# Optimization experiments

Hardware: AMD Instinct MI355X
Metric: run time of the kernel (lower is better)

Reference implementation:

```python
import jax, jax.numpy as jnp
from jax import lax
import numpy as np

N_BITS = 108
N_OUT = 7
# pos_bits[i, j] = bit j (MSB-first) of index i, matching `i >> (6 - j) & 1`
POS_BITS = np.array([[(i >> (6 - j)) & 1 for j in range(N_OUT)] for i in range(N_BITS)], dtype=np.float32)
# LZC value when all 108 bits are zero: 108 = 1101100b, MSB first
LZC_108 = np.array([1, 1, 0, 1, 1, 0, 0], dtype=np.float32)


def setup_inputs() -> dict:
    key = jax.random.key(0)
    # sparse binary bits so leading-zero runs are long and some rows are all-zero
    X = (jax.random.uniform(key, (2_000_000, N_BITS)) < 0.03).astype(jnp.float32)
    return {"X": X}


def _lzd(X):
    """X: [..., 108] MSB-first bits -> [..., 7] LZC MSB-first.

    Arithmetic soft-gate semantics: NOT(a)=1-a, AND(a,b)=a*b,
    OR(a,b)=a+b-a*b, MUX(s,a,b)=s*a+(1-s)*b, OR-tree = 1-prod(1-x).
    Sequential carry over `found` expressed with lax.scan (108 steps).
    """
    batch_shape = X.shape[:-1]
    bits = jnp.moveaxis(X, -1, 0)  # [108, ...]
    pos = jnp.asarray(POS_BITS, dtype=X.dtype)  # [108, 7]

    def step(carry, inp):
        found, lzc = carry                  # found: [..., 1], lzc: [..., 7]
        bit, pos_bits = inp                 # bit: [...], pos_bits: [7]
        bit = bit[..., None]                # [..., 1]
        not_found = 1.0 - found             # NOT
        is_first = bit * not_found          # AND
        # MUX per output bit: is_first ? pos_bit : lzc
        lzc = is_first * pos_bits + (1.0 - is_first) * lzc
        # OR: found | is_first
        found = found + is_first - found * is_first
        return (found, lzc), None

    found0 = jnp.zeros(batch_shape + (1,), X.dtype)
    lzc0 = jnp.zeros(batch_shape + (N_OUT,), X.dtype)
    (found, lzc), _ = lax.scan(step, (found0, lzc0), (bits, pos))

    # OR-tree over all 108 bits, then all-zero override with LZC=108
    any_one = 1.0 - jnp.prod(1.0 - X, axis=-1, keepdims=True)  # [..., 1]
    all_zero = 1.0 - any_one                                   # NOT
    lzc108 = jnp.asarray(LZC_108, dtype=X.dtype)               # [7]
    return all_zero * lzc108 + (1.0 - all_zero) * lzc


def reference(X):
    return _lzd(X)
```

## Files before the change

### kernel.cpp

```cpp
#include <hip/hip_runtime.h>


#define LZD_NBITS 108
#define LZD_NOUT 7

__global__ __launch_bounds__(256) void lzd108_kernel(const float* __restrict__ X,
                                                     float* __restrict__ out,
                                                     int n_rows) {
    int row = blockIdx.x * blockDim.x + threadIdx.x;
    if (row >= n_rows) return;

    const float4* p = reinterpret_cast<const float4*>(X + (size_t)row * LZD_NBITS);

    int idx = -1;

    #pragma unroll 1
    for (int c = 0; c < 6; ++c) {
        float4 v0 = p[4 * c + 0];
        float4 v1 = p[4 * c + 1];
        float4 v2 = p[4 * c + 2];
        float4 v3 = p[4 * c + 3];
        unsigned m = 0u;
        m |= (v0.x != 0.0f) ? (1u << 0)  : 0u;
        m |= (v0.y != 0.0f) ? (1u << 1)  : 0u;
        m |= (v0.z != 0.0f) ? (1u << 2)  : 0u;
        m |= (v0.w != 0.0f) ? (1u << 3)  : 0u;
        m |= (v1.x != 0.0f) ? (1u << 4)  : 0u;
        m |= (v1.y != 0.0f) ? (1u << 5)  : 0u;
        m |= (v1.z != 0.0f) ? (1u << 6)  : 0u;
        m |= (v1.w != 0.0f) ? (1u << 7)  : 0u;
        m |= (v2.x != 0.0f) ? (1u << 8)  : 0u;
        m |= (v2.y != 0.0f) ? (1u << 9)  : 0u;
        m |= (v2.z != 0.0f) ? (1u << 10) : 0u;
        m |= (v2.w != 0.0f) ? (1u << 11) : 0u;
        m |= (v3.x != 0.0f) ? (1u << 12) : 0u;
        m |= (v3.y != 0.0f) ? (1u << 13) : 0u;
        m |= (v3.z != 0.0f) ? (1u << 14) : 0u;
        m |= (v3.w != 0.0f) ? (1u << 15) : 0u;
        if (m) {
            idx = 16 * c + (__ffs(m) - 1);
            break;
        }
    }

    if (idx < 0) {
        float4 v0 = p[24];
        float4 v1 = p[25];
        float4 v2 = p[26];
        unsigned m = 0u;
        m |= (v0.x != 0.0f) ? (1u << 0)  : 0u;
        m |= (v0.y != 0.0f) ? (1u << 1)  : 0u;
        m |= (v0.z != 0.0f) ? (1u << 2)  : 0u;
        m |= (v0.w != 0.0f) ? (1u << 3)  : 0u;
        m |= (v1.x != 0.0f) ? (1u << 4)  : 0u;
        m |= (v1.y != 0.0f) ? (1u << 5)  : 0u;
        m |= (v1.z != 0.0f) ? (1u << 6)  : 0u;
        m |= (v1.w != 0.0f) ? (1u << 7)  : 0u;
        m |= (v2.x != 0.0f) ? (1u << 8)  : 0u;
        m |= (v2.y != 0.0f) ? (1u << 9)  : 0u;
        m |= (v2.z != 0.0f) ? (1u << 10) : 0u;
        m |= (v2.w != 0.0f) ? (1u << 11) : 0u;
        idx = m ? (96 + (__ffs(m) - 1)) : LZD_NBITS;
    }

    float* o = out + (size_t)row * LZD_NOUT;
    o[0] = (float)((idx >> 6) & 1);
    o[1] = (float)((idx >> 5) & 1);
    o[2] = (float)((idx >> 4) & 1);
    o[3] = (float)((idx >> 3) & 1);
    o[4] = (float)((idx >> 2) & 1);
    o[5] = (float)((idx >> 1) & 1);
    o[6] = (float)(idx & 1);
}

extern "C" void kernel_launch(void* const* d_in, const int* in_sizes, int n_in,
                              void* d_out, int out_size, void* d_ws, size_t ws_size,
                              hipStream_t stream) {
    const float* X = (const float*)d_in[0];
    float* out = (float*)d_out;
    int n_rows = in_sizes[0] / LZD_NBITS;
    int block = 256;
    int grid = (n_rows + block - 1) / block;
    lzd108_kernel<<<grid, block, 0, stream>>>(X, out, n_rows);
}
```

Baseline: 1.027 ms.

## Coalesce row loads via block-cooperative float4 reads and shared-memory key reduction

Each block now reads its 256 rows as one contiguous stream of float4s, so adjacent threads load adjacent addresses. Each float4 is turned into a 16-bit first-set-position key in shared memory, and each thread then takes the minimum over its row's 27 keys. The old version had each thread stride through its own row with early exit, which gave uncoalesced access. The new version gives up early exit and always reads all 108 bits, in exchange for full coalescing.

New measurement: 1.116 ms. +8.7%, slower.

```diff
diff --git a/kernel.cpp b/kernel.cpp
--- a/kernel.cpp
+++ b/kernel.cpp
@@ -3,74 +3,79 @@
 
 #define LZD_NBITS 108
 #define LZD_NOUT 7
+#define RPB 256
+#define F4R 27
+#define F4B (RPB * F4R)
+#define KPAD 28
+
+static __device__ __forceinline__ unsigned umin_(unsigned a, unsigned b) {
+    return a < b ? a : b;
+}
 
 __global__ __launch_bounds__(256) void lzd108_kernel(const float* __restrict__ X,
                                                      float* __restrict__ out,
                                                      int n_rows) {
-    int row = blockIdx.x * blockDim.x + threadIdx.x;
-    if (row >= n_rows) return;
+    __shared__ unsigned short keys[RPB][KPAD];
+    const int tid = threadIdx.x;
+    const size_t row0 = (size_t)blockIdx.x * RPB;
+    const float4* __restrict__ p =
+        reinterpret_cast<const float4*>(X) + row0 * F4R;
 
-    const float4* p = reinterpret_cast<const float4*>(X + (size_t)row * LZD_NBITS);
+    keys[tid][F4R] = (unsigned short)0xFFFFu;
 
-    int idx = -1;
+    const size_t nf4_rem = ((size_t)n_rows - row0) * F4R;
 
-    #pragma unroll 1
-    for (int c = 0; c < 6; ++c) {
-        float4 v0 = p[4 * c + 0];
-        float4 v1 = p[4 * c + 1];
-        float4 v2 = p[4 * c + 2];
-        float4 v3 = p[4 * c + 3];
-        unsigned m = 0u;
-        m |= (v0.x != 0.0f) ? (1u << 0)  : 0u;
-        m |= (v0.y != 0.0f) ? (1u << 1)  : 0u;
-        m |= (v0.z != 0.0f) ? (1u << 2)  : 0u;
-        m |= (v0.w != 0.0f) ? (1u << 3)  : 0u;
-        m |= (v1.x != 0.0f) ? (1u << 4)  : 0u;
-        m |= (v1.y != 0.0f) ? (1u << 5)  : 0u;
-        m |= (v1.z != 0.0f) ? (1u << 6)  : 0u;
-        m |= (v1.w != 0.0f) ? (1u << 7)  : 0u;
-        m |= (v2.x != 0.0f) ? (1u << 8)  : 0u;
-        m |= (v2.y != 0.0f) ? (1u << 9)  : 0u;
-        m |= (v2.z != 0.0f) ? (1u << 10) : 0u;
-        m |= (v2.w != 0.0f) ? (1u << 11) : 0u;
-        m |= (v3.x != 0.0f) ? (1u << 12) : 0u;
-        m |= (v3.y != 0.0f) ? (1u << 13) : 0u;
-        m |= (v3.z != 0.0f) ? (1u << 14) : 0u;
-        m |= (v3.w != 0.0f) ? (1u << 15) : 0u;
-        if (m) {
-            idx = 16 * c + (__ffs(m) - 1);
-            break;
+    if (nf4_rem >= (size_t)F4B) {
+        #pragma unroll
+        for (int it = 0; it < F4B / RPB; ++it) {
+            const int i = tid + it * RPB;
+            const float4 v = p[i];
+            const int r = i / F4R;
+            const int c = i - r * F4R;
+            const unsigned sub = (v.x != 0.0f) ? 0u
+                               : (v.y != 0.0f) ? 1u
+                               : (v.z != 0.0f) ? 2u
+                               : (v.w != 0.0f) ? 3u : 4u;
+            keys[r][c] = (sub == 4u) ? (unsigned short)0xFFFFu
+                                     : (unsigned short)(4u * (unsigned)c + sub);
+        }
+    } else {
+        const int nf4 = (int)nf4_rem;
+        #pragma unroll 1
+        for (int i = tid; i < nf4; i += RPB) {
+            const float4 v = p[i];
+            const int r = i / F4R;
+            const int c = i - r * F4R;
+            const unsigned sub = (v.x != 0.0f) ? 0u
+                               : (v.y != 0.0f) ? 1u
+                               : (v.z != 0.0f) ? 2u
+                               : (v.w != 0.0f) ? 3u : 4u;
+            keys[r][c] = (sub == 4u) ? (unsigned short)0xFFFFu
+                                     : (unsigned short)(4u * (unsigned)c + sub);
         }
     }
+    __syncthreads();
 
-    if (idx < 0) {
-        float4 v0 = p[24];
-        float4 v1 = p[25];
-        float4 v2 = p[26];
-        unsigned m = 0u;
-        m |= (v0.x != 0.0f) ? (1u << 0)  : 0u;
-        m |= (v0.y != 0.0f) ? (1u << 1)  : 0u;
-        m |= (v0.z != 0.0f) ? (1u << 2)  : 0u;
-        m |= (v0.w != 0.0f) ? (1u << 3)  : 0u;
-        m |= (v1.x != 0.0f) ? (1u << 4)  : 0u;
-        m |= (v1.y != 0.0f) ? (1u << 5)  : 0u;
-        m |= (v1.z != 0.0f) ? (1u << 6)  : 0u;
-        m |= (v1.w != 0.0f) ? (1u << 7)  : 0u;
-        m |= (v2.x != 0.0f) ? (1u << 8)  : 0u;
-        m |= (v2.y != 0.0f) ? (1u << 9)  : 0u;
-        m |= (v2.z != 0.0f) ? (1u << 10) : 0u;
-        m |= (v2.w != 0.0f) ? (1u << 11) : 0u;
-        idx = m ? (96 + (__ffs(m) - 1)) : LZD_NBITS;
+    const size_t row = row0 + (size_t)tid;
+    if (row < (size_t)n_rows) {
+        const uint2* kp = reinterpret_cast<const uint2*>(&keys[tid][0]);
+        unsigned m = 0xFFFFu;
+        #pragma unroll
+        for (int j = 0; j < 7; ++j) {
+            const uint2 u = kp[j];
+            m = umin_(m, umin_(umin_(u.x & 0xFFFFu, u.x >> 16),
+                               umin_(u.y & 0xFFFFu, u.y >> 16)));
+        }
+        const unsigned idx = (m > 107u) ? (unsigned)LZD_NBITS : m;
+        float* o = out + row * LZD_NOUT;
+        o[0] = (float)((idx >> 6) & 1u);
+        o[1] = (float)((idx >> 5) & 1u);
+        o[2] = (float)((idx >> 4) & 1u);
+        o[3] = (float)((idx >> 3) & 1u);
+        o[4] = (float)((idx >> 2) & 1u);
+        o[5] = (float)((idx >> 1) & 1u);
+        o[6] = (float)(idx & 1u);
     }
-
-    float* o = out + (size_t)row * LZD_NOUT;
-    o[0] = (float)((idx >> 6) & 1);
-    o[1] = (float)((idx >> 5) & 1);
-    o[2] = (float)((idx >> 4) & 1);
-    o[3] = (float)((idx >> 3) & 1);
-    o[4] = (float)((idx >> 2) & 1);
-    o[5] = (float)((idx >> 1) & 1);
-    o[6] = (float)(idx & 1);
 }
 
 extern "C" void kernel_launch(void* const* d_in, const int* in_sizes, int n_in,
@@ -80,6 +85,6 @@
     float* out = (float*)d_out;
     int n_rows = in_sizes[0] / LZD_NBITS;
     int block = 256;
-    int grid = (n_rows + block - 1) / block;
+    int grid = (n_rows + RPB - 1) / RPB;
     lzd108_kernel<<<grid, block, 0, stream>>>(X, out, n_rows);
 }
```

## Issue 16 aligned 128B-segment loads upfront and extract bits from exponent

Applied to the files above, without the earlier changes.

Each thread now aligns its row pointer down to a 128-byte boundary and issues 16 uint4 loads at once instead of a serial early-exit loop of 4-load chunks. Nonzero detection reads one exponent bit of each float, which assumes the inputs are exactly 0.0 or 1.0. A 64-bit mask is built and scanned with ctz, with the remaining words loaded only when the first 256 bytes hold no set bit. This raises memory-level parallelism and cuts per-load latency chains, but adds register pressure and possibly wasted bytes read for rows with an early hit.

Result: slower. 1.060 ms (+3.3%).

```diff
diff --git a/kernel.cpp b/kernel.cpp
--- a/kernel.cpp
+++ b/kernel.cpp
@@ -4,66 +4,59 @@
 #define LZD_NBITS 108
 #define LZD_NOUT 7
 
+static __device__ __forceinline__ unsigned nib(uint4 w) {
+    return (w.x >> 23 & 1u) | (w.y >> 22 & 2u) |
+           (w.z >> 21 & 4u) | (w.w >> 20 & 8u);
+}
+
 __global__ __launch_bounds__(256) void lzd108_kernel(const float* __restrict__ X,
                                                      float* __restrict__ out,
                                                      int n_rows) {
-    int row = blockIdx.x * blockDim.x + threadIdx.x;
-    if (row >= n_rows) return;
+    const int r = blockIdx.x * blockDim.x + threadIdx.x;
+    if (r >= n_rows) return;
 
-    const float4* p = reinterpret_cast<const float4*>(X + (size_t)row * LZD_NBITS);
+    const unsigned off = (108u * (unsigned)r) & 31u;
+    const uint4* __restrict__ P =
+        reinterpret_cast<const uint4*>(X + (size_t)r * 108u - off);
 
-    int idx = -1;
+    uint4 a[16];
+    #pragma unroll
+    for (int q = 0; q < 16; ++q) a[q] = P[q];
 
-    #pragma unroll 1
-    for (int c = 0; c < 6; ++c) {
-        float4 v0 = p[4 * c + 0];
-        float4 v1 = p[4 * c + 1];
-        float4 v2 = p[4 * c + 2];
-        float4 v3 = p[4 * c + 3];
-        unsigned m = 0u;
-        m |= (v0.x != 0.0f) ? (1u << 0)  : 0u;
-        m |= (v0.y != 0.0f) ? (1u << 1)  : 0u;
-        m |= (v0.z != 0.0f) ? (1u << 2)  : 0u;
-        m |= (v0.w != 0.0f) ? (1u << 3)  : 0u;
-        m |= (v1.x != 0.0f) ? (1u << 4)  : 0u;
-        m |= (v1.y != 0.0f) ? (1u << 5)  : 0u;
-        m |= (v1.z != 0.0f) ? (1u << 6)  : 0u;
-        m |= (v1.w != 0.0f) ? (1u << 7)  : 0u;
-        m |= (v2.x != 0.0f) ? (1u << 8)  : 0u;
-        m |= (v2.y != 0.0f) ? (1u << 9)  : 0u;
-        m |= (v2.z != 0.0f) ? (1u << 10) : 0u;
-        m |= (v2.w != 0.0f) ? (1u << 11) : 0u;
-        m |= (v3.x != 0.0f) ? (1u << 12) : 0u;
-        m |= (v3.y != 0.0f) ? (1u << 13) : 0u;
-        m |= (v3.z != 0.0f) ? (1u << 14) : 0u;
-        m |= (v3.w != 0.0f) ? (1u << 15) : 0u;
-        if (m) {
-            idx = 16 * c + (__ffs(m) - 1);
-            break;
+    unsigned long long mA = 0ull;
+    #pragma unroll
+    for (int q = 0; q < 16; ++q)
+        mA |= (unsigned long long)nib(a[q]) << (4 * q);
+    mA &= (~0ull) << off;
+
+    int epos;
+    if (mA) {
+        epos = __builtin_ctzll(mA);
+    } else {
+        unsigned long long mB = 0ull;
+        unsigned mC = 0u;
+        #pragma unroll
+        for (int q = 16; q <= 26; ++q) {
+            mB |= (unsigned long long)nib(P[q]) << (4 * (q - 16));
         }
+        #pragma unroll
+        for (int q = 27; q <= 31; ++q) {
+            if (off >= 4u * (unsigned)q - 104u)
+                mB |= (unsigned long long)nib(P[q]) << (4 * (q - 16));
+        }
+        #pragma unroll
+        for (int q = 32; q <= 33; ++q) {
+            if (off >= 4u * (unsigned)q - 104u)
+                mC |= nib(P[q]) << (4 * (q - 32));
+        }
+        if (mB)       epos = 64 + __builtin_ctzll(mB);
+        else if (mC)  epos = 128 + __builtin_ctz(mC);
+        else          epos = -1;
     }
 
-    if (idx < 0) {
-        float4 v0 = p[24];
-        float4 v1 = p[25];
-        float4 v2 = p[26];
-        unsigned m = 0u;
-        m |= (v0.x != 0.0f) ? (1u << 0)  : 0u;
-        m |= (v0.y != 0.0f) ? (1u << 1)  : 0u;
-        m |= (v0.z != 0.0f) ? (1u << 2)  : 0u;
-        m |= (v0.w != 0.0f) ? (1u << 3)  : 0u;
-        m |= (v1.x != 0.0f) ? (1u << 4)  : 0u;
-        m |= (v1.y != 0.0f) ? (1u << 5)  : 0u;
-        m |= (v1.z != 0.0f) ? (1u << 6)  : 0u;
-        m |= (v1.w != 0.0f) ? (1u << 7)  : 0u;
-        m |= (v2.x != 0.0f) ? (1u << 8)  : 0u;
-        m |= (v2.y != 0.0f) ? (1u << 9)  : 0u;
-        m |= (v2.z != 0.0f) ? (1u << 10) : 0u;
-        m |= (v2.w != 0.0f) ? (1u << 11) : 0u;
-        idx = m ? (96 + (__ffs(m) - 1)) : LZD_NBITS;
-    }
+    const int idx = (epos < 0) ? LZD_NBITS : (epos - (int)off);
 
-    float* o = out + (size_t)row * LZD_NOUT;
+    float* o = out + (size_t)r * LZD_NOUT;
     o[0] = (float)((idx >> 6) & 1);
     o[1] = (float)((idx >> 5) & 1);
     o[2] = (float)((idx >> 4) & 1);
```
